# Kernel tuning notes

Measured on AMD Instinct MI355X. Metric: run time of the kernel, lower is better.

Reference implementation:

```python
import jax, jax.numpy as jnp
import numpy as np

HEADS = 16
DIM_HEAD = 64
SCALE = DIM_HEAD ** -0.5
EPS = 1e-5


def layer_norm(x, gamma):
    mu = jnp.mean(x, axis=-1, keepdims=True)
    var = jnp.var(x, axis=-1, keepdims=True)
    return (x - mu) * jax.lax.rsqrt(var + EPS) * gamma


def setup_inputs() -> dict:
    key = jax.random.key(0)
    ks = jax.random.split(key, 5)
    B, S, D = 2, 2048, 1024
    x = jax.random.normal(ks[0], (B, S, D), dtype=jnp.float32)
    gamma = jnp.ones((D,), dtype=jnp.float32)
    Wq = jax.random.normal(ks[1], (D, HEADS * DIM_HEAD), dtype=jnp.float32) * (D ** -0.5)
    Wkv = jax.random.normal(ks[2], (D, 2 * DIM_HEAD), dtype=jnp.float32) * (D ** -0.5)
    Wo = jax.random.normal(ks[3], (HEADS * DIM_HEAD, D), dtype=jnp.float32) * ((HEADS * DIM_HEAD) ** -0.5)
    return {"x": x, "gamma": gamma, "Wq": Wq, "Wkv": Wkv, "Wo": Wo}


def reference(x, gamma, Wq, Wkv, Wo):
    B, S, D = x.shape
    kv_input = x  # context=None -> self attention
    xn = layer_norm(x, gamma)
    q = xn @ Wq                          # [B,S,H*Dh]
    kv = kv_input @ Wkv                  # [B,S,2*Dh]
    k, v = jnp.split(kv, 2, axis=-1)     # each [B,S,Dh]
    q = q.reshape(B, S, HEADS, DIM_HEAD).transpose(0, 2, 1, 3) * SCALE  # [B,H,S,Dh]
    sim = jnp.einsum('bhid,bjd->bhij', q, k)  # [B,H,S,S]
    # causal mask: triu(j - i + 1) masked
    i_idx = jnp.arange(S)[:, None]
    j_idx = jnp.arange(S)[None, :]
    neg = -jnp.finfo(sim.dtype).max
    sim = jnp.where(j_idx > i_idx, neg, sim)
    attn = jax.nn.softmax(sim, axis=-1)
    out = jnp.einsum('bhij,bjd->bhid', attn, v)  # [B,H,S,Dh]
    out = out.transpose(0, 2, 1, 3).reshape(B, S, HEADS * DIM_HEAD)
    return out @ Wo
```

## Files before the change

### kernel.cpp

```cpp
#include <hip/hip_runtime.h>

typedef unsigned short u16;
typedef __attribute__((ext_vector_type(8))) u16    u16x8;
typedef __attribute__((ext_vector_type(4))) u16    u16x4;
typedef __attribute__((ext_vector_type(2))) unsigned u32x2;
typedef __attribute__((ext_vector_type(8))) __bf16 bf16x8;
typedef __attribute__((ext_vector_type(4))) float  f32x4;
typedef __attribute__((ext_vector_type(16))) float f32x16;

__device__ __forceinline__ u16 f2bf(float f) {
    unsigned u = __float_as_uint(f);
    u += 0x7fffu + ((u >> 16) & 1u);
    return (u16)(u >> 16);
}
__device__ __forceinline__ bf16x8 ldbf8(const u16* p) {
    return __builtin_bit_cast(bf16x8, *(const u16x8*)p);
}
__device__ __forceinline__ f32x4 mfma16(bf16x8 a, bf16x8 b, f32x4 c) {
    return __builtin_amdgcn_mfma_f32_16x16x32_bf16(a, b, c, 0, 0, 0);
}
__device__ __forceinline__ f32x16 mfma32x(bf16x8 a, bf16x8 b, f32x16 c) {
    return __builtin_amdgcn_mfma_f32_32x32x16_bf16(a, b, c, 0, 0, 0);
}
__device__ __forceinline__ float exp2a(float x) {
    float r; asm("v_exp_f32 %0, %1" : "=v"(r) : "v"(x)); return r;
}
__device__ __forceinline__ unsigned cvtpk(float lo, float hiv) {
    unsigned r; asm("v_cvt_pk_bf16_f32 %0, %1, %2" : "=v"(r) : "v"(lo), "v"(hiv)); return r;
}
__device__ __forceinline__ u32x2 permswap2(unsigned a, unsigned b) {
    return __builtin_amdgcn_permlane32_swap(a, b, false, false);
}
__device__ __forceinline__ float combine_sum(float x) {
    u32x2 pr = permswap2(__float_as_uint(x), __float_as_uint(x));
    return __uint_as_float(pr[0]) + __uint_as_float(pr[1]);
}
__device__ __forceinline__ bf16x8 pack4(unsigned a, unsigned b, unsigned c, unsigned d) {
    union { unsigned u[4]; bf16x8 v; } t; t.u[0] = a; t.u[1] = b; t.u[2] = c; t.u[3] = d; return t.v;
}

__global__ void transpose_cast_all(const float* __restrict__ Wq, const float* __restrict__ Wkv,
                                   const float* __restrict__ Wo, u16* __restrict__ Wq_t,
                                   u16* __restrict__ Wkv_t, u16* __restrict__ Wo_t, float qscale) {
    __shared__ float tile[32][33];
    int by = blockIdx.y;
    const float* W; u16* Wt; int N; float scale;
    if (by < 32)      { W = Wq;  Wt = Wq_t;  N = 1024; scale = qscale; }
    else if (by < 36) { W = Wkv; Wt = Wkv_t; N = 128;  by -= 32; scale = 1.0f; }
    else              { W = Wo;  Wt = Wo_t;  N = 1024; by -= 36; scale = 1.0f; }
    const int K = 1024;
    int kb = blockIdx.x * 32, nb = by * 32;
    int tx = threadIdx.x, ty = threadIdx.y;
#pragma unroll
    for (int i = 0; i < 32; i += 8)
        tile[ty + i][tx] = W[(size_t)(kb + ty + i) * N + nb + tx];
    __syncthreads();
#pragma unroll
    for (int i = 0; i < 32; i += 8)
        Wt[(size_t)(nb + ty + i) * K + kb + tx] = f2bf(tile[tx][ty + i] * scale);
}

__global__ __launch_bounds__(256) void ln_cast(const float* __restrict__ x, const float* __restrict__ gamma,
                                               u16* __restrict__ xn, u16* __restrict__ xb) {
    const int row = blockIdx.x;
    const int t = threadIdx.x;
    const float4 v = ((const float4*)(x + (size_t)row * 1024))[t];
    float s  = v.x + v.y + v.z + v.w;
    float s2 = v.x * v.x + v.y * v.y + v.z * v.z + v.w * v.w;
#pragma unroll
    for (int off = 32; off; off >>= 1) { s += __shfl_down(s, off); s2 += __shfl_down(s2, off); }
    __shared__ float red[2][4];
    const int w = t >> 6, lane = t & 63;
    if (lane == 0) { red[0][w] = s; red[1][w] = s2; }
    __syncthreads();
    s  = red[0][0] + red[0][1] + red[0][2] + red[0][3];
    s2 = red[1][0] + red[1][1] + red[1][2] + red[1][3];
    const float mu  = s * (1.0f / 1024.0f);
    const float var = s2 * (1.0f / 1024.0f) - mu * mu;
    const float rs  = rsqrtf(var + 1e-5f);
    const float4 g = ((const float4*)gamma)[t];
    u16x4 on, ob;
    on.x = f2bf((v.x - mu) * rs * g.x); on.y = f2bf((v.y - mu) * rs * g.y);
    on.z = f2bf((v.z - mu) * rs * g.z); on.w = f2bf((v.w - mu) * rs * g.w);
    ob.x = f2bf(v.x); ob.y = f2bf(v.y); ob.z = f2bf(v.z); ob.w = f2bf(v.w);
    ((u16x4*)(xn + (size_t)row * 1024))[t] = on;
    ((u16x4*)(xb + (size_t)row * 1024))[t] = ob;
}

template<int BM, int BN, int EPI>
__global__ __launch_bounds__(256, 2) void gemm_bt(const u16* __restrict__ A, const u16* __restrict__ Bt,
                                                  u16* __restrict__ Cb, float* __restrict__ Cf,
                                                  u16* __restrict__ Cv, int M, int N, int K) {
    constexpr int WM = BM / 2, WN = BN / 2, FM = WM / 16, FN = WN / 16;
    constexpr int CHA = BM * 4, CH = (BM + BN) * 4, ITERS = CH / 256;
    __shared__ __align__(16) u16 lds[2][(BM + BN) * 32];
    const int tid = threadIdx.x;
    const int m0 = blockIdx.x * BM, n0 = blockIdx.y * BN;
    const int w = tid >> 6, lane = tid & 63, cl = lane & 15, kg = lane >> 4;
    const int wr = w >> 1, wc = w & 1;

    auto stage = [&](int buf, int k0) {
#pragma unroll
        for (int it = 0; it < ITERS; ++it) {
            int c = it * 256 + tid;
            const u16* g;
            if (c < CHA) { int r = c >> 2, cc = c & 3; g = A  + (size_t)(m0 + r) * K + k0 + cc * 8; }
            else { int c2 = c - CHA; int r = c2 >> 2, cc = c2 & 3; g = Bt + (size_t)(n0 + r) * K + k0 + cc * 8; }
            __builtin_amdgcn_global_load_lds(
                (const __attribute__((address_space(1))) unsigned int*)g,
                (__attribute__((address_space(3))) unsigned int*)&lds[buf][c * 8], 16, 0, 0);
        }
    };

    const f32x4 zero = {0.f, 0.f, 0.f, 0.f};
    f32x4 acc[FM][FN];
#pragma unroll
    for (int m = 0; m < FM; m++)
#pragma unroll
        for (int n = 0; n < FN; n++) acc[m][n] = zero;

    const int KT = K / 32;
    stage(0, 0);
    for (int t = 0; t < KT; ++t) {
        __syncthreads();
        if (t + 1 < KT) stage((t + 1) & 1, (t + 1) * 32);
        const u16* As = &lds[t & 1][0];
        const u16* Bs = &lds[t & 1][BM * 32];
        bf16x8 af[FM], bfr[FN];
#pragma unroll
        for (int m = 0; m < FM; m++) af[m]  = ldbf8(As + (wr * WM + m * 16 + cl) * 32 + kg * 8);
#pragma unroll
        for (int n = 0; n < FN; n++) bfr[n] = ldbf8(Bs + (wc * WN + n * 16 + cl) * 32 + kg * 8);
#pragma unroll
        for (int m = 0; m < FM; m++)
#pragma unroll
            for (int n = 0; n < FN; n++) acc[m][n] = mfma16(af[m], bfr[n], acc[m][n]);
    }

#pragma unroll
    for (int m = 0; m < FM; m++)
#pragma unroll
        for (int n = 0; n < FN; n++)
#pragma unroll
            for (int r = 0; r < 4; r++) {
                const int row = m0 + wr * WM + m * 16 + kg * 4 + r;
                const int col = n0 + wc * WN + n * 16 + cl;
                const float v = acc[m][n][r];
                if constexpr (EPI == 0) Cb[(size_t)row * N + col] = f2bf(v);
                else if constexpr (EPI == 1) Cf[(size_t)row * N + col] = v;
                else {
                    if (col < 64) Cb[(size_t)row * 64 + col] = f2bf(v);
                    else { int bb = row >> 11, s = row & 2047;
                           Cv[((size_t)bb * 64 + (col - 64)) * 2048 + s] = f2bf(v); }
                }
            }
}

__global__ __launch_bounds__(256) void kmax_kernel(const u16* __restrict__ kb, float* __restrict__ kpart) {
    const int b = blockIdx.x >> 5, blk = blockIdx.x & 31;
    const int tid = threadIdx.x;
    const int r = blk * 64 + (tid >> 2), c4 = tid & 3;
    const u16* kp = kb + ((size_t)b * 2048 + r) * 64 + c4 * 16;
    float s2 = 0.f;
#pragma unroll
    for (int i = 0; i < 2; i++) {
        u16x8 v = ((const u16x8*)kp)[i];
#pragma unroll
        for (int j = 0; j < 8; j++) {
            const float f = __uint_as_float(((unsigned)v[j]) << 16);
            s2 = fmaf(f, f, s2);
        }
    }
    s2 += __shfl_xor(s2, 1); s2 += __shfl_xor(s2, 2);
    float mx = s2;
#pragma unroll
    for (int off = 4; off < 64; off <<= 1) mx = fmaxf(mx, __shfl_xor(mx, off));
    __shared__ float red[4];
    if ((tid & 63) == 0) red[tid >> 6] = mx;
    __syncthreads();
    if (tid == 0)
        kpart[blockIdx.x] = fmaxf(fmaxf(red[0], red[1]), fmaxf(red[2], red[3]));
}

__global__ __launch_bounds__(256, 2) void attn_fwd(const u16* __restrict__ q, const u16* __restrict__ k,
                                                   const u16* __restrict__ vt, const float* __restrict__ kpart,
                                                   u16* __restrict__ o) {
    constexpr int S = 2048;
    const int bid = blockIdx.x;
    const int p = (bid < 256) ? (bid >> 5) : (15 - ((bid - 256) >> 5));
    const int bh = bid & 31;
    const int h = bh & 15, b = bh >> 4;
    const int tid = threadIdx.x, w = tid >> 6, lane = tid & 63;
    const int pw = w & 1, par = w >> 1;
    const int l31 = lane & 31;
    const bool hi = (lane & 32) != 0;
    const int hi1 = hi ? 1 : 0, hi8 = hi ? 8 : 0;
    const int t1 = 2 * p + pw, t2 = 63 - t1;
    const int iters = 32 - p;
    const size_t bS = (size_t)b * S;

    __shared__ __align__(16) u16 smem[18432];

    auto stageK = [&](int jt, int buf, int tl) {
        const int r = tid >> 3, c = tid & 7;
        const u16* gp = k + (bS + jt * 32 + r) * 64 + ((c ^ (r & 7)) * 8);
        __builtin_amdgcn_global_load_lds(
            (const __attribute__((address_space(1))) unsigned int*)gp,
            (__attribute__((address_space(3))) unsigned int*)(smem + (buf * 2 + tl) * 2048 + tid * 8), 16, 0, 0);
    };
    auto loadV = [&](int jt) -> u16x8 {
        const int rv = tid >> 2, c4 = tid & 3;
        return *(const u16x8*)(vt + ((size_t)b * 64 + rv) * S + jt * 32 + c4 * 8);
    };
    auto writeV = [&](int buf, int tl, u16x8 v) {
        const int rv = tid >> 2, c4 = tid & 3;
        *(u16x8*)(smem + 8192 + (buf * 2 + tl) * 2560 + rv * 40 + c4 * 8) = v;
    };

    float km = kpart[(b << 5) + l31];
#pragma unroll
    for (int off = 1; off < 32; off <<= 1) km = fmaxf(km, __shfl_xor(km, off));
    const float kmaxb = sqrtf(km);

    bf16x8 qf1[4], qf2[4];
    float mB1, mB2;
    auto qload = [&](int t, bf16x8 (&qf)[4]) -> float {
        const u16* qp = q + (bS + t * 32 + l31) * 1024 + h * 64 + hi8;
        float qn2 = 0.f;
#pragma unroll
        for (int sub = 0; sub < 4; sub++) {
            qf[sub] = ldbf8(qp + sub * 16);
            const u16x8 uv = __builtin_bit_cast(u16x8, qf[sub]);
#pragma unroll
            for (int j = 0; j < 8; j++) {
                const float v = __uint_as_float(((unsigned)uv[j]) << 16);
                qn2 = fmaf(v, v, qn2);
            }
        }
        return sqrtf(combine_sum(qn2)) * kmaxb;
    };
    mB1 = qload(t1, qf1);
    mB2 = qload(t2, qf2);

    f32x16 a1lo, a1hi, a2lo, a2hi;
#pragma unroll
    for (int r = 0; r < 16; r++) { a1lo[r] = 0.f; a1hi[r] = 0.f; a2lo[r] = 0.f; a2hi[r] = 0.f; }
    float l1 = 0.f, l2 = 0.f;

    auto process = [&](const bf16x8 (&qf)[4], const bf16x8 (&kf)[4],
                       const bf16x8& vf00, const bf16x8& vf01, const bf16x8& vf10, const bf16x8& vf11,
                       f32x16& a0, f32x16& a1, float& lr, float mB, bool diag) {
        f32x16 s;
#pragma unroll
        for (int r = 0; r < 16; r++) s[r] = 0.f;
#pragma unroll
        for (int sub = 0; sub < 4; sub++) s = mfma32x(kf[sub], qf[sub], s);
        if (diag) {
#pragma unroll
            for (int r = 0; r < 16; r++) {
                const int kvl = (r & 3) + 8 * (r >> 2) + (hi ? 4 : 0);
                if (kvl > l31) s[r] = -1e30f;
            }
        }
        float p0 = 0.f, p1 = 0.f;
#pragma unroll
        for (int r = 0; r < 16; r += 2) {
            const float ea = exp2a(s[r] - mB);
            const float eb = exp2a(s[r + 1] - mB);
            s[r] = ea; s[r + 1] = eb;
            p0 += ea; p1 += eb;
        }
        lr += p0 + p1;
        unsigned w0 = cvtpk(s[0], s[1]),  w1 = cvtpk(s[2], s[3]);
        unsigned w2 = cvtpk(s[4], s[5]),  w3 = cvtpk(s[6], s[7]);
        u32x2 r02 = permswap2(w0, w2), r13 = permswap2(w1, w3);
        bf16x8 pf0 = pack4(r02[0], r13[0], r02[1], r13[1]);
        unsigned y0 = cvtpk(s[8], s[9]),   y1 = cvtpk(s[10], s[11]);
        unsigned y2 = cvtpk(s[12], s[13]), y3 = cvtpk(s[14], s[15]);
        u32x2 t02 = permswap2(y0, y2), t13 = permswap2(y1, y3);
        bf16x8 pf1 = pack4(t02[0], t13[0], t02[1], t13[1]);
        a0 = mfma32x(vf00, pf0, a0);
        a0 = mfma32x(vf01, pf1, a0);
        a1 = mfma32x(vf10, pf0, a1);
        a1 = mfma32x(vf11, pf1, a1);
    };

    stageK(0, 0, 0); stageK(1, 0, 1);
    u16x8 v0 = loadV(0), v1 = loadV(1);
    for (int i = 0; i < iters; i++) {
        const int buf = i & 1;
        writeV(buf, 0, v0); writeV(buf, 1, v1);
        __syncthreads();
        if (i + 1 < iters) {
            stageK(2 * i + 2, buf ^ 1, 0); stageK(2 * i + 3, buf ^ 1, 1);
            v0 = loadV(2 * i + 2); v1 = loadV(2 * i + 3);
        }
        const int jt = 2 * i + par;
        if (jt <= t2) {
            const u16* kcur = smem + (buf * 2 + par) * 2048;
            const u16* vcur = smem + 8192 + (buf * 2 + par) * 2560;
            bf16x8 kf[4];
#pragma unroll
            for (int sub = 0; sub < 4; sub++)
                kf[sub] = ldbf8(kcur + l31 * 64 + (((sub * 2 + hi1) ^ (l31 & 7)) * 8));
            const bf16x8 vf00 = ldbf8(vcur + l31 * 40 + hi8);
            const bf16x8 vf01 = ldbf8(vcur + l31 * 40 + 16 + hi8);
            const bf16x8 vf10 = ldbf8(vcur + (32 + l31) * 40 + hi8);
            const bf16x8 vf11 = ldbf8(vcur + (32 + l31) * 40 + 16 + hi8);
            if (jt <= t1) process(qf1, kf, vf00, vf01, vf10, vf11, a1lo, a1hi, l1, mB1, jt == t1);
            process(qf2, kf, vf00, vf01, vf10, vf11, a2lo, a2hi, l2, mB2, jt == t2);
        }
    }
    float l1t = combine_sum(l1), l2t = combine_sum(l2);

    float* fm = (float*)smem;
    __syncthreads();
    {
        float* dst = fm + (((pw * 2) + (par ? 0 : 1)) * 64 + lane) * 36;
        if (par) { *(f32x16*)dst = a1lo; *(f32x16*)(dst + 16) = a1hi; dst[32] = l1t; }
        else     { *(f32x16*)dst = a2lo; *(f32x16*)(dst + 16) = a2hi; dst[32] = l2t; }
    }
    __syncthreads();
    {
        const float* src = fm + (((pw * 2) + (par ? 1 : 0)) * 64 + lane) * 36;
        const f32x16 s0 = *(const f32x16*)src;
        const f32x16 s1 = *(const f32x16*)(src + 16);
        if (par) {
#pragma unroll
            for (int r = 0; r < 16; r++) { a2lo[r] += s0[r]; a2hi[r] += s1[r]; }
            l2t += src[32];
        } else {
#pragma unroll
            for (int r = 0; r < 16; r++) { a1lo[r] += s0[r]; a1hi[r] += s1[r]; }
            l1t += src[32];
        }
    }
    __syncthreads();

    auto epi = [&](const f32x16& a0, const f32x16& a1, float lt, int t) {
        const float rl = 1.0f / lt;
        u16* lb = smem + w * 2304;
#pragma unroll
        for (int i = 0; i < 8; i++) {
            const int d = ((2 * i) & 3) + 8 * ((2 * i) >> 2) + (hi ? 4 : 0);
            *(unsigned*)&lb[l31 * 72 + d]      = cvtpk(a0[2 * i] * rl, a0[2 * i + 1] * rl);
            *(unsigned*)&lb[l31 * 72 + 32 + d] = cvtpk(a1[2 * i] * rl, a1[2 * i + 1] * rl);
        }
        asm volatile("s_waitcnt lgkmcnt(0)" ::: "memory");
#pragma unroll
        for (int i = 0; i < 4; i++) {
            const int qq = i * 8 + (lane >> 3), dd = (lane & 7) * 8;
            *(u16x8*)(o + (bS + t * 32 + qq) * 1024 + h * 64 + dd) = *(const u16x8*)&lb[qq * 72 + dd];
        }
    };
    if (par == 0) epi(a1lo, a1hi, l1t, t1);
    else          epi(a2lo, a2hi, l2t, t2);
}

extern "C" void kernel_launch(void* const* d_in, const int* in_sizes, int n_in,
                              void* d_out, int out_size, void* d_ws, size_t ws_size,
                              hipStream_t stream) {
    const float* x     = (const float*)d_in[0];
    const float* gamma = (const float*)d_in[1];
    const float* Wq    = (const float*)d_in[2];
    const float* Wkv   = (const float*)d_in[3];
    const float* Wo    = (const float*)d_in[4];
    float* out = (float*)d_out;
    char* ws = (char*)d_ws;

    u16* Wq_t  = (u16*)(ws + 0);
    u16* Wo_t  = (u16*)(ws + (2u << 20));
    u16* Wkv_t = (u16*)(ws + (4u << 20));
    u16* xn    = (u16*)(ws + 4456448u);
    u16* xb    = (u16*)(ws + 12845056u);
    u16* qb    = (u16*)(ws + 21233664u);
    u16* kb    = (u16*)(ws + 29622272u);
    u16* vtb   = (u16*)(ws + 30146560u);
    u16* attb  = (u16*)(ws + 30670848u);
    float* kpart = (float*)xb;

    const float qscale = 0.125f * 1.44269504f;
    transpose_cast_all<<<dim3(32, 68), dim3(32, 8), 0, stream>>>(Wq, Wkv, Wo, Wq_t, Wkv_t, Wo_t, qscale);

    ln_cast<<<4096, 256, 0, stream>>>(x, gamma, xn, xb);

    gemm_bt<128, 64, 0><<<dim3(32, 16), 256, 0, stream>>>(xn, Wq_t, qb, nullptr, nullptr, 4096, 1024, 1024);
    gemm_bt<64, 64, 2><<<dim3(64, 2), 256, 0, stream>>>(xb, Wkv_t, kb, nullptr, vtb, 4096, 128, 1024);
    kmax_kernel<<<64, 256, 0, stream>>>(kb, kpart);
    attn_fwd<<<512, 256, 0, stream>>>(qb, kb, vtb, kpart, attb);
    gemm_bt<128, 64, 1><<<dim3(32, 16), 256, 0, stream>>>(attb, Wo_t, nullptr, out, nullptr, 4096, 1024, 1024);
}
```

Measured before the change: 94.42 us.

## Widen GEMM K-tile with XOR swizzle, remap blocks, fuse K-norm max into KV GEMM

The GEMM template gains a BK parameter, and the Q and output projections now use 64-wide K tiles. Global-to-LDS chunks are placed with an XOR swizzle so the MFMA fragment reads hit fewer LDS bank conflicts. Workgroup IDs are remapped in interleaved groups of eight to change which tiles run together for cache locality. The separate kmax kernel is removed, and the KV GEMM epilogue now computes the per-block max squared key norm, saving one launch and one pass over K at the cost of doubling LDS per block for the wider tiles.

```diff
diff --git a/kernel.cpp b/kernel.cpp
--- a/kernel.cpp
+++ b/kernel.cpp
@@ -87,15 +87,22 @@
     ((u16x4*)(xb + (size_t)row * 1024))[t] = ob;
 }
 
-template<int BM, int BN, int EPI>
+template<int BM, int BN, int BK, int EPI>
 __global__ __launch_bounds__(256, 2) void gemm_bt(const u16* __restrict__ A, const u16* __restrict__ Bt,
                                                   u16* __restrict__ Cb, float* __restrict__ Cf,
                                                   u16* __restrict__ Cv, int M, int N, int K) {
     constexpr int WM = BM / 2, WN = BN / 2, FM = WM / 16, FN = WN / 16;
-    constexpr int CHA = BM * 4, CH = (BM + BN) * 4, ITERS = CH / 256;
-    __shared__ __align__(16) u16 lds[2][(BM + BN) * 32];
+    constexpr int CPR = BK / 8;
+    constexpr int MS = CPR - 1;
+    constexpr int CHA = BM * CPR, CH = (BM + BN) * CPR, ITERS = CH / 256;
+    __shared__ __align__(16) u16 lds[2][(BM + BN) * BK];
+    __shared__ float kred[2][64];
     const int tid = threadIdx.x;
-    const int m0 = blockIdx.x * BM, n0 = blockIdx.y * BN;
+    const int nwg = gridDim.x * gridDim.y;
+    int lin = blockIdx.x + gridDim.x * blockIdx.y;
+    lin = (lin & 7) * (nwg >> 3) + (lin >> 3);
+    const int bx = lin % gridDim.x, by = lin / gridDim.x;
+    const int m0 = bx * BM, n0 = by * BN;
     const int w = tid >> 6, lane = tid & 63, cl = lane & 15, kg = lane >> 4;
     const int wr = w >> 1, wc = w & 1;
 
@@ -104,8 +111,8 @@
         for (int it = 0; it < ITERS; ++it) {
             int c = it * 256 + tid;
             const u16* g;
-            if (c < CHA) { int r = c >> 2, cc = c & 3; g = A  + (size_t)(m0 + r) * K + k0 + cc * 8; }
-            else { int c2 = c - CHA; int r = c2 >> 2, cc = c2 & 3; g = Bt + (size_t)(n0 + r) * K + k0 + cc * 8; }
+            if (c < CHA) { int r = c / CPR, cc = c & MS; g = A  + (size_t)(m0 + r) * K + k0 + ((cc ^ (r & MS)) * 8); }
+            else { int c2 = c - CHA; int r = c2 / CPR, cc = c2 & MS; g = Bt + (size_t)(n0 + r) * K + k0 + ((cc ^ (r & MS)) * 8); }
             __builtin_amdgcn_global_load_lds(
                 (const __attribute__((address_space(1))) unsigned int*)g,
                 (__attribute__((address_space(3))) unsigned int*)&lds[buf][c * 8], 16, 0, 0);
@@ -119,22 +126,31 @@
 #pragma unroll
         for (int n = 0; n < FN; n++) acc[m][n] = zero;
 
-    const int KT = K / 32;
+    const int KT = K / BK;
     stage(0, 0);
     for (int t = 0; t < KT; ++t) {
         __syncthreads();
-        if (t + 1 < KT) stage((t + 1) & 1, (t + 1) * 32);
+        if (t + 1 < KT) stage((t + 1) & 1, (t + 1) * BK);
         const u16* As = &lds[t & 1][0];
-        const u16* Bs = &lds[t & 1][BM * 32];
-        bf16x8 af[FM], bfr[FN];
-#pragma unroll
-        for (int m = 0; m < FM; m++) af[m]  = ldbf8(As + (wr * WM + m * 16 + cl) * 32 + kg * 8);
-#pragma unroll
-        for (int n = 0; n < FN; n++) bfr[n] = ldbf8(Bs + (wc * WN + n * 16 + cl) * 32 + kg * 8);
-#pragma unroll
-        for (int m = 0; m < FM; m++)
-#pragma unroll
-            for (int n = 0; n < FN; n++) acc[m][n] = mfma16(af[m], bfr[n], acc[m][n]);
+        const u16* Bs = &lds[t & 1][BM * BK];
+#pragma unroll
+        for (int s = 0; s < BK / 32; s++) {
+            bf16x8 af[FM], bfr[FN];
+#pragma unroll
+            for (int m = 0; m < FM; m++) {
+                const int ra = wr * WM + m * 16 + cl;
+                af[m] = ldbf8(As + ra * BK + (((s * 4 + kg) ^ (ra & MS)) * 8));
+            }
+#pragma unroll
+            for (int n = 0; n < FN; n++) {
+                const int rb = wc * WN + n * 16 + cl;
+                bfr[n] = ldbf8(Bs + rb * BK + (((s * 4 + kg) ^ (rb & MS)) * 8));
+            }
+#pragma unroll
+            for (int m = 0; m < FM; m++)
+#pragma unroll
+                for (int n = 0; n < FN; n++) acc[m][n] = mfma16(af[m], bfr[n], acc[m][n]);
+        }
     }
 
 #pragma unroll
@@ -154,32 +170,42 @@
                            Cv[((size_t)bb * 64 + (col - 64)) * 2048 + s] = f2bf(v); }
                 }
             }
-}
-
-__global__ __launch_bounds__(256) void kmax_kernel(const u16* __restrict__ kb, float* __restrict__ kpart) {
-    const int b = blockIdx.x >> 5, blk = blockIdx.x & 31;
-    const int tid = threadIdx.x;
-    const int r = blk * 64 + (tid >> 2), c4 = tid & 3;
-    const u16* kp = kb + ((size_t)b * 2048 + r) * 64 + c4 * 16;
-    float s2 = 0.f;
-#pragma unroll
-    for (int i = 0; i < 2; i++) {
-        u16x8 v = ((const u16x8*)kp)[i];
-#pragma unroll
-        for (int j = 0; j < 8; j++) {
-            const float f = __uint_as_float(((unsigned)v[j]) << 16);
-            s2 = fmaf(f, f, s2);
+
+    if constexpr (EPI == 2) {
+        if (n0 == 0) {
+            float s2[FM][4];
+#pragma unroll
+            for (int m = 0; m < FM; m++)
+#pragma unroll
+                for (int r = 0; r < 4; r++) {
+                    float t = 0.f;
+#pragma unroll
+                    for (int n = 0; n < FN; n++) {
+                        const float vb = __uint_as_float(((unsigned)f2bf(acc[m][n][r])) << 16);
+                        t = fmaf(vb, vb, t);
+                    }
+                    s2[m][r] = t;
+                }
+#pragma unroll
+            for (int off = 1; off < 16; off <<= 1)
+#pragma unroll
+                for (int m = 0; m < FM; m++)
+#pragma unroll
+                    for (int r = 0; r < 4; r++) s2[m][r] += __shfl_xor(s2[m][r], off);
+            if (cl == 0)
+#pragma unroll
+                for (int m = 0; m < FM; m++)
+#pragma unroll
+                    for (int r = 0; r < 4; r++) kred[wc][wr * 32 + m * 16 + kg * 4 + r] = s2[m][r];
+            __syncthreads();
+            if (tid < 64) {
+                float t = kred[0][tid] + kred[1][tid];
+#pragma unroll
+                for (int off = 1; off < 64; off <<= 1) t = fmaxf(t, __shfl_xor(t, off));
+                if (tid == 0) Cf[bx] = t;
+            }
         }
     }
-    s2 += __shfl_xor(s2, 1); s2 += __shfl_xor(s2, 2);
-    float mx = s2;
-#pragma unroll
-    for (int off = 4; off < 64; off <<= 1) mx = fmaxf(mx, __shfl_xor(mx, off));
-    __shared__ float red[4];
-    if ((tid & 63) == 0) red[tid >> 6] = mx;
-    __syncthreads();
-    if (tid == 0)
-        kpart[blockIdx.x] = fmaxf(fmaxf(red[0], red[1]), fmaxf(red[2], red[3]));
 }
 
 __global__ __launch_bounds__(256, 2) void attn_fwd(const u16* __restrict__ q, const u16* __restrict__ k,
@@ -384,9 +410,8 @@
 
     ln_cast<<<4096, 256, 0, stream>>>(x, gamma, xn, xb);
 
-    gemm_bt<128, 64, 0><<<dim3(32, 16), 256, 0, stream>>>(xn, Wq_t, qb, nullptr, nullptr, 4096, 1024, 1024);
-    gemm_bt<64, 64, 2><<<dim3(64, 2), 256, 0, stream>>>(xb, Wkv_t, kb, nullptr, vtb, 4096, 128, 1024);
-    kmax_kernel<<<64, 256, 0, stream>>>(kb, kpart);
+    gemm_bt<128, 64, 64, 0><<<dim3(32, 16), 256, 0, stream>>>(xn, Wq_t, qb, nullptr, nullptr, 4096, 1024, 1024);
+    gemm_bt<64, 64, 32, 2><<<dim3(64, 2), 256, 0, stream>>>(xb, Wkv_t, kb, kpart, vtb, 4096, 128, 1024);
     attn_fwd<<<512, 256, 0, stream>>>(qb, kb, vtb, kpart, attb);
-    gemm_bt<128, 64, 1><<<dim3(32, 16), 256, 0, stream>>>(attb, Wo_t, nullptr, out, nullptr, 4096, 1024, 1024);
-}
+    gemm_bt<128, 64, 64, 1><<<dim3(32, 16), 256, 0, stream>>>(attb, Wo_t, nullptr, out, nullptr, 4096, 1024, 1024);
+}
```

Measured after the change: 94.45 us. About the same (+0.0%).
